# Kernel optimization log

Hardware: AMD Instinct MI355X
Metric: run time of the kernel (lower is better)

Reference implementation:

```python
import jax, jax.numpy as jnp
import numpy as np

N, D, H1, K = 4096, 128, 256, 128


def setup_inputs() -> dict:
    key = jax.random.key(0)
    ks = jax.random.split(key, 8)
    A = jax.random.uniform(ks[3], (D, D), dtype=jnp.float32)
    A = A * (1.0 - jnp.eye(D, dtype=jnp.float32))  # DAG prob mask, no self-loops
    return {
        "x": jax.random.normal(ks[0], (N, D), dtype=jnp.float32),
        "weight": jax.random.normal(ks[1], (D, D), dtype=jnp.float32) * 0.1,
        "bias": jax.random.normal(ks[2], (1, D), dtype=jnp.float32) * 0.1,
        "A": A,
        "W1": jax.random.normal(ks[4], (D, H1), dtype=jnp.float32) * 0.1,
        "b1": jax.random.normal(ks[5], (H1,), dtype=jnp.float32) * 0.1,
        "W2": jax.random.normal(ks[6], (H1, K), dtype=jnp.float32) * 0.1,
        "b2": jax.random.normal(ks[7], (K,), dtype=jnp.float32) * 0.1,
    }


def reference(x, weight, bias, A, W1, b1, W2, b2):
    # to_adj (eval path): masked weights
    W = weight * A                                   # [D, D]
    y = x @ W + bias                                 # [N, D]
    # __expand__ builds diag(y[n]) [N,D,D]; since e[n,i,:] = y[n,i]*I[i,:],
    # the first Linear collapses to a per-row scaling of W1 (same math, fused):
    # e @ W1 -> y[n,i] * W1[i,:]
    h1 = jax.nn.relu(y[:, :, None] * W1[None, :, :] + b1)   # [N, D, H1]
    f = (h1 @ W2 + b2).sum(axis=2)                   # [N, D] (sum over output dim)
    # h_func, method='gnn'
    I = jnp.eye(D, dtype=x.dtype)
    A2 = jnp.square(W)
    M = I + A2 / D
    E = jnp.linalg.matrix_power(M, D - 1)
    h_val = (E.T * M).sum() - D
    # l1_reg (same prob mask in eval)
    reg = jnp.abs(W).sum()
    return (f, h_val, reg)
```

## Files before the change

kernel.cpp:

```cpp
#include <hip/hip_runtime.h>

#define NN 4096
#define DD 128
#define HH1 256

#define WS_S    0
#define WS_S2   16384
#define WS_S3   32768
#define WS_S4   49152
#define WS_W    65536
#define WS_W2S  81920
#define WS_PAIR 82176
#define WS_B2S  82688
#define WS_TACC 82696
#define WS_DONE 82708
#define WS_REGP 82712
#define WS_WT   82944
#define WS_XT   99328
#define WS_TH   623616
#define WS_A    656384
#define WS_B    689280
#define WS_REQ_FLOATS 722176
#define WS_REQ_BYTES  (WS_REQ_FLOATS * 4UL)

#define O_S    0
#define O_S2   16384
#define O_S3   32768
#define O_S4   49152
#define O_W2S  65536
#define O_B2S  65792
#define O_TACC 65808
#define O_DONE 65824
#define O_REGP 65840

__device__ __forceinline__ float waveReduce(float v) {
#pragma unroll
  for (int off = 32; off > 0; off >>= 1) v += __shfl_down(v, off, 64);
  return v;
}


__global__ __launch_bounds__(256) void kA2(
    const float* __restrict__ weight, const float* __restrict__ Amat,
    const float* __restrict__ W2, const float* __restrict__ b2,
    const float* __restrict__ b1v, const float* __restrict__ x,
    float* __restrict__ ws) {
  const int b = blockIdx.x, tid = threadIdx.x;
  __shared__ float s_lds[DD * DD];
  __shared__ float xs[64 * 133];
  if (b < 64) {
    const float4* w4 = (const float4*)weight;
    const float4* a4 = (const float4*)Amat;
    float4* s4 = (float4*)s_lds;
    const float inv = 1.0f / 128.0f;
    for (int e = tid; e < DD * DD / 4; e += 256) {
      float4 wv = w4[e], av = a4[e], o;
      float t;
      t = wv.x * av.x; o.x = t * t * inv;
      t = wv.y * av.y; o.y = t * t * inv;
      t = wv.z * av.z; o.z = t * t * inv;
      t = wv.w * av.w; o.w = t * t * inv;
      s4[e] = o;
    }
    __syncthreads();
    const int i = (b << 1) + (tid >> 7), j = tid & 127;
    const float* row = &s_lds[i * DD];
    float acc = 0.f;
#pragma unroll 8
    for (int k = 0; k < DD; ++k) acc = fmaf(row[k], s_lds[k * DD + j], acc);
    ws[WS_S2 + i * DD + j] = acc;
  } else if (b < 72) {
    const int base = (b - 64) * 2048;
    const float inv = 1.0f / 128.0f;
    for (int e = tid; e < 2048; e += 256) {
      const int idx = base + e;
      const float w = weight[idx] * Amat[idx];
      const int k = idx >> 7, i = idx & 127;
      ws[WS_W + idx] = w;
      ws[WS_WT + i * DD + k] = w;
      ws[WS_S + idx] = w * w * inv;
    }
  } else if (b == 72) {
    const float4* r = (const float4*)(W2 + tid * 128);
    float4 s4 = make_float4(0.f, 0.f, 0.f, 0.f);
#pragma unroll 8
    for (int k = 0; k < 32; ++k) {
      const float4 v = r[k];
      s4.x += v.x; s4.y += v.y; s4.z += v.z; s4.w += v.w;
    }
    const float w2sv = (s4.x + s4.y) + (s4.z + s4.w);
    ws[WS_W2S + tid] = w2sv;
    ((float2*)(ws + WS_PAIR))[tid] = make_float2(b1v[tid], w2sv);
  } else if (b == 73) {
    __shared__ float red[4];
    float v = (tid < 128) ? b2[tid] : 0.f;
    v = waveReduce(v);
    if ((tid & 63) == 0) red[tid >> 6] = v;
    __syncthreads();
    if (tid == 0) ws[WS_B2S] = (red[0] + red[1]) + (red[2] + red[3]);
    if (tid >= 64 && tid < 74) ws[WS_TACC + (tid - 64)] = 0.f;
    if (tid == 96) *(unsigned int*)(ws + WS_DONE) = 0u;
  } else if (b < 82) {
    const int bb = b - 74;
    const int base = bb * 2048;
    float s = 0.f;
    for (int e = tid; e < 2048; e += 256) {
      const int idx = base + e;
      s += fabsf(weight[idx] * Amat[idx]);
    }
    s = waveReduce(s);
    __shared__ float red2[4];
    if ((tid & 63) == 0) red2[tid >> 6] = s;
    __syncthreads();
    if (tid == 0) ws[WS_REGP + bb] = (red2[0] + red2[1]) + (red2[2] + red2[3]);
  } else {
    const int n0 = (b - 82) * 64;
    const float4* x4 = (const float4*)x;
    for (int e = tid; e < 2048; e += 256) {
      const int r = e >> 5, c = e & 31;
      const float4 v = x4[(n0 + r) * 32 + c];
      float* p = &xs[r * 133 + (c << 2)];
      p[0] = v.x; p[1] = v.y; p[2] = v.z; p[3] = v.w;
    }
    __syncthreads();
    float* xT = ws + WS_XT;
    const int c = tid & 15, ks = tid >> 4;
#pragma unroll
    for (int m = 0; m < 8; ++m) {
      const int k = ks + (m << 4);
      float4 o;
      o.x = xs[((c << 2) + 0) * 133 + k];
      o.y = xs[((c << 2) + 1) * 133 + k];
      o.z = xs[((c << 2) + 2) * 133 + k];
      o.w = xs[((c << 2) + 3) * 133 + k];
      *(float4*)&xT[k * NN + n0 + (c << 2)] = o;
    }
  }
}

__global__ __launch_bounds__(256) void kPS(const float* __restrict__ W1,
                                           const float* __restrict__ b1v,
                                           float* __restrict__ ws) {
  const int tid = threadIdx.x;
  if (blockIdx.x < 128) {
    const int sb = blockIdx.x;
    const bool isS4 = sb >= 64;
    const int mb = isS4 ? sb - 64 : sb;
    const float* __restrict__ L = ws + WS_S2;
    const float* __restrict__ R = ws + (isS4 ? WS_S2 : WS_S);
    float* __restrict__ O = ws + (isS4 ? WS_S4 : WS_S3);
    const int i = (mb << 1) + (tid >> 7), j = tid & 127;
    float acc = 0.f;
#pragma unroll 8
    for (int k = 0; k < DD; ++k) acc = fmaf(L[i * DD + k], R[k * DD + j], acc);
    O[i * DD + j] = acc;
    return;
  }
  const int i = blockIdx.x - 128;
  __shared__ float kT[256], kS[256], kC[256];
  __shared__ float redb[8];
  __shared__ float base2[2];
  const int j = tid;
  const float w = W1[i * HH1 + j];
  const float w2s = ws[WS_W2S + j];
  const float bj = b1v[j];
  const float s = w * w2s, c = bj * w2s;
  float th, ds, dc, bs, bc;
  if (w > 0.f) {
    th = -bj / w; ds = s; dc = c; bs = 0.f; bc = 0.f;
  } else if (w < 0.f) {
    th = -bj / w; ds = -s; dc = -c; bs = s; bc = c;
  } else {
    th = 3.4e38f; ds = 0.f; dc = 0.f; bs = 0.f; bc = fmaxf(bj, 0.f) * w2s;
  }
  {
    const float rs = waveReduce(bs), rc = waveReduce(bc);
    if ((tid & 63) == 0) {
      redb[tid >> 6] = rs;
      redb[4 + (tid >> 6)] = rc;
    }
  }
  kT[tid] = th; kS[tid] = ds; kC[tid] = dc;
  __syncthreads();
  if (tid == 0) {
    base2[0] = (redb[0] + redb[1]) + (redb[2] + redb[3]);
    base2[1] = (redb[4] + redb[5]) + (redb[6] + redb[7]);
  }
  for (int kk = 2; kk <= 256; kk <<= 1) {
    for (int jj = kk >> 1; jj > 0; jj >>= 1) {
      __syncthreads();
      const int ixj = tid ^ jj;
      if (ixj > tid) {
        const bool up = ((tid & kk) == 0);
        const float ta = kT[tid], tb = kT[ixj];
        if ((ta > tb) == up) {
          kT[tid] = tb; kT[ixj] = ta;
          const float sa = kS[tid], sb = kS[ixj];
          kS[tid] = sb; kS[ixj] = sa;
          const float ca = kC[tid], cb = kC[ixj];
          kC[tid] = cb; kC[ixj] = ca;
        }
      }
    }
  }
  __syncthreads();
  for (int off = 1; off < 256; off <<= 1) {
    float vs = 0.f, vc = 0.f;
    if (tid >= off) { vs = kS[tid - off]; vc = kC[tid - off]; }
    __syncthreads();
    kS[tid] += vs; kC[tid] += vc;
    __syncthreads();
  }
  const float b_s = base2[0], b_c = base2[1];
  ws[WS_TH + i * 256 + tid] = kT[tid];
  ws[WS_A + i * 257 + tid + 1] = b_s + kS[tid];
  ws[WS_B + i * 257 + tid + 1] = b_c + kC[tid];
  if (tid == 0) {
    ws[WS_A + i * 257] = b_s;
    ws[WS_B + i * 257] = b_c;
  }
}

__global__ __launch_bounds__(256) void kC6(const float* __restrict__ bias,
                                           float* __restrict__ ws,
                                           float* __restrict__ out) {
  const int tid = threadIdx.x;
  if (blockIdx.x < 512) {
    __shared__ float lT[4 * 256];
    __shared__ float lA[4 * 257];
    __shared__ float lB[4 * 257];
    __shared__ float ts[256 * 5];
    const int fb = blockIdx.x;
    const int n0 = (fb >> 5) << 8, i0 = (fb & 31) << 2;
    const int w = tid >> 6, l = tid & 63;
    const int iu = __builtin_amdgcn_readfirstlane(i0 + w);

#pragma unroll
    for (int q = 0; q < 4; ++q) {
      lT[(q << 8) + tid] = ws[WS_TH + (i0 + q) * 256 + tid];
      lA[q * 257 + tid] = ws[WS_A + (i0 + q) * 257 + tid];
      lB[q * 257 + tid] = ws[WS_B + (i0 + q) * 257 + tid];
      if (tid == 0) {
        lA[q * 257 + 256] = ws[WS_A + (i0 + q) * 257 + 256];
        lB[q * 257 + 256] = ws[WS_B + (i0 + q) * 257 + 256];
      }
    }

    const float* __restrict__ xT = ws + WS_XT;
    const float* __restrict__ wr = ws + WS_WT + iu * DD;
    float t[4] = {0.f, 0.f, 0.f, 0.f};
#pragma unroll 8
    for (int k = 0; k < DD; ++k) {
      const float wv = wr[k];
      const float4 xv = *(const float4*)&xT[k * NN + n0 + (l << 2)];
      t[0] = fmaf(xv.x, wv, t[0]);
      t[1] = fmaf(xv.y, wv, t[1]);
      t[2] = fmaf(xv.z, wv, t[2]);
      t[3] = fmaf(xv.w, wv, t[3]);
    }
    const float bv = bias[iu];
    const float sb2 = ws[WS_B2S];
    __syncthreads();

    const float* Tw = &lT[w << 8];
    const float* Aw = &lA[w * 257];
    const float* Bw = &lB[w * 257];
#pragma unroll
    for (int q = 0; q < 4; ++q) {
      const float yq = t[q] + bv;
      int m = 0;
#pragma unroll
      for (int st = 128; st > 0; st >>= 1) {
        if (Tw[m + st - 1] <= yq) m += st;
      }
      const float f = fmaf(Aw[m], yq, Bw[m]) + sb2;
      ts[((l << 2) + q) * 5 + w] = f;
    }
    __syncthreads();
    const int m = tid;
    float4 o;
    o.x = ts[m * 5 + 0]; o.y = ts[m * 5 + 1];
    o.z = ts[m * 5 + 2]; o.w = ts[m * 5 + 3];
    *(float4*)&out[(n0 + m) * DD + i0] = o;
    return;
  }
  const int tb = blockIdx.x - 512;
  const int i = (tb << 1) + (tid >> 7), j = tid & 127;
  const float* S1 = ws + WS_S;
  const float* S2 = ws + WS_S2;
  const float* S3 = ws + WS_S3;
  const float* S4 = ws + WS_S4;
  const float a1 = S1[i * DD + j], a2 = S2[i * DD + j], a3 = S3[i * DD + j];
  const float b1t = S1[j * DD + i], b2t = S2[j * DD + i],
              b3t = S3[j * DD + i], b4t = S4[j * DD + i];
  float e7 = 0.f;
#pragma unroll 8
  for (int k = 0; k < DD; ++k) e7 = fmaf(S3[i * DD + k], S4[k * DD + j], e7);
  float c[10];
  c[0] = a1 * b1t; c[1] = a2 * b1t; c[2] = a2 * b2t; c[3] = a3 * b2t;
  c[4] = a3 * b3t; c[5] = a3 * b4t; c[6] = e7 * b1t; c[7] = e7 * b2t;
  c[8] = e7 * b3t; c[9] = e7 * b4t;
  __shared__ float red[4][10];
#pragma unroll
  for (int m = 0; m < 10; ++m) {
    const float v = waveReduce(c[m]);
    if ((tid & 63) == 0) red[tid >> 6][m] = v;
  }
  __syncthreads();
  if (tid == 0) {
    float* tacc = ws + WS_TACC;
    for (int m = 0; m < 10; ++m)
      atomicAdd(&tacc[m], (red[0][m] + red[1][m]) + (red[2][m] + red[3][m]));
    __threadfence();
    unsigned int* done = (unsigned int*)(ws + WS_DONE);
    const unsigned int old = atomicAdd(done, 1u);
    if (old == 63u) {
      __threadfence();
      double h = 0.0, C = 8128.0;
      for (int kk = 2; kk <= 11; ++kk) {
        const float tv = atomicAdd(&tacc[kk - 2], 0.0f);
        h += C * (double)tv;
        C = C * (double)(128 - kk) / (double)(kk + 1);
      }
      float reg = 0.f;
      for (int m = 0; m < 8; ++m) reg += ws[WS_REGP + m];
      out[NN * DD] = (float)h;
      out[NN * DD + 1] = reg;
    }
  }
}

__global__ __launch_bounds__(256) void kA_old(
    const float* __restrict__ weight, const float* __restrict__ Amat,
    const float* __restrict__ W2, const float* __restrict__ b2,
    float* __restrict__ ws) {
  const int b = blockIdx.x, tid = threadIdx.x;
  if (b < 64) {
    __shared__ float s_lds[DD * DD];
    const float4* w4 = (const float4*)weight;
    const float4* a4 = (const float4*)Amat;
    float4* s4 = (float4*)s_lds;
    const float inv = 1.0f / 128.0f;
    for (int e = tid; e < DD * DD / 4; e += 256) {
      float4 wv = w4[e], av = a4[e], o;
      float t;
      t = wv.x * av.x; o.x = t * t * inv;
      t = wv.y * av.y; o.y = t * t * inv;
      t = wv.z * av.z; o.z = t * t * inv;
      t = wv.w * av.w; o.w = t * t * inv;
      s4[e] = o;
    }
    __syncthreads();
    const int i = (b << 1) + (tid >> 7), j = tid & 127;
    const float* row = &s_lds[i * DD];
    float acc = 0.f;
#pragma unroll 8
    for (int k = 0; k < DD; ++k) acc = fmaf(row[k], s_lds[k * DD + j], acc);
    ws[O_S2 + i * DD + j] = acc;
  } else if (b < 72) {
    const int base = (b - 64) * 2048;
    const float inv = 1.0f / 128.0f;
    for (int e = tid; e < 2048; e += 256) {
      const int idx = base + e;
      const float w = weight[idx] * Amat[idx];
      ws[O_S + idx] = w * w * inv;
    }
  } else if (b == 72) {
    const float4* r = (const float4*)(W2 + tid * 128);
    float4 s4 = make_float4(0.f, 0.f, 0.f, 0.f);
#pragma unroll 8
    for (int k = 0; k < 32; ++k) {
      const float4 v = r[k];
      s4.x += v.x; s4.y += v.y; s4.z += v.z; s4.w += v.w;
    }
    ws[O_W2S + tid] = (s4.x + s4.y) + (s4.z + s4.w);
  } else if (b == 73) {
    __shared__ float red[4];
    float v = (tid < 128) ? b2[tid] : 0.f;
    v = waveReduce(v);
    if ((tid & 63) == 0) red[tid >> 6] = v;
    __syncthreads();
    if (tid == 0) ws[O_B2S] = (red[0] + red[1]) + (red[2] + red[3]);
    if (tid >= 64 && tid < 74) ws[O_TACC + (tid - 64)] = 0.f;
    if (tid == 96) *(unsigned int*)(ws + O_DONE) = 0u;
  } else {
    const int bb = b - 74;
    const int base = bb * 2048;
    float s = 0.f;
    for (int e = tid; e < 2048; e += 256) {
      const int idx = base + e;
      s += fabsf(weight[idx] * Amat[idx]);
    }
    s = waveReduce(s);
    __shared__ float red[4];
    if ((tid & 63) == 0) red[tid >> 6] = s;
    __syncthreads();
    if (tid == 0) ws[O_REGP + bb] = (red[0] + red[1]) + (red[2] + red[3]);
  }
}

__global__ __launch_bounds__(256) void kB_old(
    const float* __restrict__ x, const float* __restrict__ weight,
    const float* __restrict__ Amat, const float* __restrict__ bias,
    const float* __restrict__ W1, const float* __restrict__ b1v,
    float* __restrict__ ws, float* __restrict__ out) {
  const int tid = threadIdx.x;
  if (blockIdx.x < 128) {
    const int sb = blockIdx.x;
    const bool isS4 = sb >= 64;
    const int mb = isS4 ? sb - 64 : sb;
    const float* __restrict__ L = ws + O_S2;
    const float* __restrict__ R = ws + (isS4 ? O_S2 : O_S);
    float* __restrict__ O = ws + (isS4 ? O_S4 : O_S3);
    const int i = (mb << 1) + (tid >> 7), j = tid & 127;
    float acc = 0.f;
#pragma unroll 8
    for (int k = 0; k < DD; ++k) acc = fmaf(L[i * DD + k], R[k * DD + j], acc);
    O[i * DD + j] = acc;
    return;
  }
  __shared__ float xs[64 * 132];
  __shared__ float4 fq[4 * 256];
  __shared__ float wcol[4 * 128];
  __shared__ float ts[64 * 5];
  const int fb = blockIdx.x - 128;
  const int i0 = (fb & 31) << 2, n0 = (fb >> 5) << 6;
  const float4* x4 = (const float4*)x;
  for (int e = tid; e < 64 * 32; e += 256) {
    const int r = e >> 5, c = e & 31;
    *(float4*)&xs[r * 132 + (c << 2)] = x4[(n0 + r) * 32 + c];
  }
  for (int e = tid; e < 512; e += 256) {
    const int w = e >> 7, k = e & 127;
    const int gi = k * DD + i0 + w;
    wcol[(w << 7) + k] = weight[gi] * Amat[gi];
  }
  const float* w2s = ws + O_W2S;
  for (int e = tid; e < 1024; e += 256) {
    const int w = e >> 8, j = e & 255;
    fq[(w << 8) + j] = make_float4(W1[(i0 + w) * HH1 + j], b1v[j], w2s[j], 0.f);
  }
  __syncthreads();
  const int w = tid >> 6, l = tid & 63;
  float t = bias[i0 + w];
  const float4* xr = (const float4*)&xs[l * 132];
  const float4* wc = (const float4*)&wcol[w << 7];
#pragma unroll
  for (int k = 0; k < 32; ++k) {
    const float4 xv = xr[k], wv = wc[k];
    t = fmaf(xv.x, wv.x, t);
    t = fmaf(xv.y, wv.y, t);
    t = fmaf(xv.z, wv.z, t);
    t = fmaf(xv.w, wv.w, t);
  }
  float acc = ws[O_B2S];
  const float4* fp = &fq[w << 8];
#pragma unroll 8
  for (int j = 0; j < HH1; ++j) {
    const float4 c = fp[j];
    acc = fmaf(fmaxf(fmaf(t, c.x, c.y), 0.f), c.z, acc);
  }
  ts[l * 5 + w] = acc;
  __syncthreads();
  if (tid < 64) {
    const float4 o = make_float4(ts[tid * 5 + 0], ts[tid * 5 + 1],
                                 ts[tid * 5 + 2], ts[tid * 5 + 3]);
    *(float4*)&out[(n0 + tid) * DD + i0] = o;
  }
}

__global__ __launch_bounds__(256) void kC_old(float* __restrict__ ws,
                                              float* __restrict__ out) {
  const int tid = threadIdx.x;
  const int i = (blockIdx.x << 1) + (tid >> 7), j = tid & 127;
  const float* S1 = ws + O_S;
  const float* S2 = ws + O_S2;
  const float* S3 = ws + O_S3;
  const float* S4 = ws + O_S4;
  const float a1 = S1[i * DD + j], a2 = S2[i * DD + j], a3 = S3[i * DD + j];
  const float b1t = S1[j * DD + i], b2t = S2[j * DD + i],
              b3t = S3[j * DD + i], b4t = S4[j * DD + i];
  float e7 = 0.f;
#pragma unroll 8
  for (int k = 0; k < DD; ++k) e7 = fmaf(S3[i * DD + k], S4[k * DD + j], e7);
  float c[10];
  c[0] = a1 * b1t; c[1] = a2 * b1t; c[2] = a2 * b2t; c[3] = a3 * b2t;
  c[4] = a3 * b3t; c[5] = a3 * b4t; c[6] = e7 * b1t; c[7] = e7 * b2t;
  c[8] = e7 * b3t; c[9] = e7 * b4t;
  __shared__ float red[4][10];
#pragma unroll
  for (int m = 0; m < 10; ++m) {
    const float v = waveReduce(c[m]);
    if ((tid & 63) == 0) red[tid >> 6][m] = v;
  }
  __syncthreads();
  if (tid == 0) {
    float* tacc = ws + O_TACC;
    for (int m = 0; m < 10; ++m)
      atomicAdd(&tacc[m], (red[0][m] + red[1][m]) + (red[2][m] + red[3][m]));
    __threadfence();
    unsigned int* done = (unsigned int*)(ws + O_DONE);
    const unsigned int old = atomicAdd(done, 1u);
    if (old == 63u) {
      __threadfence();
      double h = 0.0, C = 8128.0;
      for (int kk = 2; kk <= 11; ++kk) {
        const float tv = atomicAdd(&tacc[kk - 2], 0.0f);
        h += C * (double)tv;
        C = C * (double)(128 - kk) / (double)(kk + 1);
      }
      float reg = 0.f;
      for (int m = 0; m < 8; ++m) reg += ws[O_REGP + m];
      out[NN * DD] = (float)h;
      out[NN * DD + 1] = reg;
    }
  }
}

extern "C" void kernel_launch(void* const* d_in, const int* in_sizes, int n_in,
                              void* d_out, int out_size, void* d_ws,
                              size_t ws_size, hipStream_t stream) {
  const float* x      = (const float*)d_in[0];
  const float* weight = (const float*)d_in[1];
  const float* bias   = (const float*)d_in[2];
  const float* Amat   = (const float*)d_in[3];
  const float* W1     = (const float*)d_in[4];
  const float* b1v    = (const float*)d_in[5];
  const float* W2     = (const float*)d_in[6];
  const float* b2     = (const float*)d_in[7];
  float* out = (float*)d_out;
  float* ws  = (float*)d_ws;

  if (ws_size >= WS_REQ_BYTES) {
    kA2<<<146, 256, 0, stream>>>(weight, Amat, W2, b2, b1v, x, ws);
    kPS<<<256, 256, 0, stream>>>(W1, b1v, ws);
    kC6<<<576, 256, 0, stream>>>(bias, ws, out);
  } else {
    kA_old<<<82, 256, 0, stream>>>(weight, Amat, W2, b2, ws);
    kB_old<<<128 + 2048, 256, 0, stream>>>(x, weight, Amat, bias, W1, b1v, ws,
                                           out);
    kC_old<<<64, 256, 0, stream>>>(ws, out);
  }
}
```

Baseline: 116.5 us.

## Move threshold sort blocks into first kernel, recomputing W2 row sums per block

The per-row threshold sort and prefix-scan blocks move from the second kernel into the first. Each block now computes the W2 row sums itself rather than reading them from workspace, so it no longer waits on a prior kernel. The second kernel keeps only the S3/S4 matrix products. The x-transpose staging buffer now reuses the shared s_lds array, which cuts the first kernel's LDS footprint. The cost is redundant W2 reads in 128 blocks and a larger first grid, with a shorter critical path in the second kernel.

```diff
diff --git a/kernel.cpp b/kernel.cpp
--- a/kernel.cpp
+++ b/kernel.cpp
@@ -40,14 +40,13 @@
 }
 
 
-__global__ __launch_bounds__(256) void kA2(
+__global__ __launch_bounds__(256) void kA3(
     const float* __restrict__ weight, const float* __restrict__ Amat,
     const float* __restrict__ W2, const float* __restrict__ b2,
     const float* __restrict__ b1v, const float* __restrict__ x,
-    float* __restrict__ ws) {
+    const float* __restrict__ W1, float* __restrict__ ws) {
   const int b = blockIdx.x, tid = threadIdx.x;
   __shared__ float s_lds[DD * DD];
-  __shared__ float xs[64 * 133];
   if (b < 64) {
     const float4* w4 = (const float4*)weight;
     const float4* a4 = (const float4*)Amat;
@@ -81,17 +80,6 @@
       ws[WS_S + idx] = w * w * inv;
     }
   } else if (b == 72) {
-    const float4* r = (const float4*)(W2 + tid * 128);
-    float4 s4 = make_float4(0.f, 0.f, 0.f, 0.f);
-#pragma unroll 8
-    for (int k = 0; k < 32; ++k) {
-      const float4 v = r[k];
-      s4.x += v.x; s4.y += v.y; s4.z += v.z; s4.w += v.w;
-    }
-    const float w2sv = (s4.x + s4.y) + (s4.z + s4.w);
-    ws[WS_W2S + tid] = w2sv;
-    ((float2*)(ws + WS_PAIR))[tid] = make_float2(b1v[tid], w2sv);
-  } else if (b == 73) {
     __shared__ float red[4];
     float v = (tid < 128) ? b2[tid] : 0.f;
     v = waveReduce(v);
@@ -100,8 +88,8 @@
     if (tid == 0) ws[WS_B2S] = (red[0] + red[1]) + (red[2] + red[3]);
     if (tid >= 64 && tid < 74) ws[WS_TACC + (tid - 64)] = 0.f;
     if (tid == 96) *(unsigned int*)(ws + WS_DONE) = 0u;
-  } else if (b < 82) {
-    const int bb = b - 74;
+  } else if (b < 81) {
+    const int bb = b - 73;
     const int base = bb * 2048;
     float s = 0.f;
     for (int e = tid; e < 2048; e += 256) {
@@ -113,8 +101,9 @@
     if ((tid & 63) == 0) red2[tid >> 6] = s;
     __syncthreads();
     if (tid == 0) ws[WS_REGP + bb] = (red2[0] + red2[1]) + (red2[2] + red2[3]);
-  } else {
-    const int n0 = (b - 82) * 64;
+  } else if (b < 145) {
+    float* xs = s_lds;
+    const int n0 = (b - 81) * 64;
     const float4* x4 = (const float4*)x;
     for (int e = tid; e < 2048; e += 256) {
       const int r = e >> 5, c = e & 31;
@@ -135,90 +124,95 @@
       o.w = xs[((c << 2) + 3) * 133 + k];
       *(float4*)&xT[k * NN + n0 + (c << 2)] = o;
     }
-  }
-}
-
-__global__ __launch_bounds__(256) void kPS(const float* __restrict__ W1,
-                                           const float* __restrict__ b1v,
-                                           float* __restrict__ ws) {
-  const int tid = threadIdx.x;
-  if (blockIdx.x < 128) {
-    const int sb = blockIdx.x;
-    const bool isS4 = sb >= 64;
-    const int mb = isS4 ? sb - 64 : sb;
-    const float* __restrict__ L = ws + WS_S2;
-    const float* __restrict__ R = ws + (isS4 ? WS_S2 : WS_S);
-    float* __restrict__ O = ws + (isS4 ? WS_S4 : WS_S3);
-    const int i = (mb << 1) + (tid >> 7), j = tid & 127;
-    float acc = 0.f;
-#pragma unroll 8
-    for (int k = 0; k < DD; ++k) acc = fmaf(L[i * DD + k], R[k * DD + j], acc);
-    O[i * DD + j] = acc;
-    return;
-  }
-  const int i = blockIdx.x - 128;
-  __shared__ float kT[256], kS[256], kC[256];
-  __shared__ float redb[8];
-  __shared__ float base2[2];
-  const int j = tid;
-  const float w = W1[i * HH1 + j];
-  const float w2s = ws[WS_W2S + j];
-  const float bj = b1v[j];
-  const float s = w * w2s, c = bj * w2s;
-  float th, ds, dc, bs, bc;
-  if (w > 0.f) {
-    th = -bj / w; ds = s; dc = c; bs = 0.f; bc = 0.f;
-  } else if (w < 0.f) {
-    th = -bj / w; ds = -s; dc = -c; bs = s; bc = c;
   } else {
-    th = 3.4e38f; ds = 0.f; dc = 0.f; bs = 0.f; bc = fmaxf(bj, 0.f) * w2s;
-  }
-  {
-    const float rs = waveReduce(bs), rc = waveReduce(bc);
-    if ((tid & 63) == 0) {
-      redb[tid >> 6] = rs;
-      redb[4 + (tid >> 6)] = rc;
-    }
-  }
-  kT[tid] = th; kS[tid] = ds; kC[tid] = dc;
-  __syncthreads();
-  if (tid == 0) {
-    base2[0] = (redb[0] + redb[1]) + (redb[2] + redb[3]);
-    base2[1] = (redb[4] + redb[5]) + (redb[6] + redb[7]);
-  }
-  for (int kk = 2; kk <= 256; kk <<= 1) {
-    for (int jj = kk >> 1; jj > 0; jj >>= 1) {
-      __syncthreads();
-      const int ixj = tid ^ jj;
-      if (ixj > tid) {
-        const bool up = ((tid & kk) == 0);
-        const float ta = kT[tid], tb = kT[ixj];
-        if ((ta > tb) == up) {
-          kT[tid] = tb; kT[ixj] = ta;
-          const float sa = kS[tid], sb = kS[ixj];
-          kS[tid] = sb; kS[ixj] = sa;
-          const float ca = kC[tid], cb = kC[ixj];
-          kC[tid] = cb; kC[ixj] = ca;
+    const int i = b - 145;
+    float* kT = s_lds;
+    float* kS = s_lds + 256;
+    float* kC = s_lds + 512;
+    __shared__ float redb[8];
+    __shared__ float base2[2];
+    const int j = tid;
+    const float4* r = (const float4*)(W2 + j * 128);
+    float4 s4v = make_float4(0.f, 0.f, 0.f, 0.f);
+#pragma unroll 8
+    for (int k = 0; k < 32; ++k) {
+      const float4 v = r[k];
+      s4v.x += v.x; s4v.y += v.y; s4v.z += v.z; s4v.w += v.w;
+    }
+    const float w2s = (s4v.x + s4v.y) + (s4v.z + s4v.w);
+    const float w = W1[i * HH1 + j];
+    const float bj = b1v[j];
+    const float s = w * w2s, c = bj * w2s;
+    float th, ds, dc, bs, bc;
+    if (w > 0.f) {
+      th = -bj / w; ds = s; dc = c; bs = 0.f; bc = 0.f;
+    } else if (w < 0.f) {
+      th = -bj / w; ds = -s; dc = -c; bs = s; bc = c;
+    } else {
+      th = 3.4e38f; ds = 0.f; dc = 0.f; bs = 0.f; bc = fmaxf(bj, 0.f) * w2s;
+    }
+    {
+      const float rs = waveReduce(bs), rc = waveReduce(bc);
+      if ((tid & 63) == 0) {
+        redb[tid >> 6] = rs;
+        redb[4 + (tid >> 6)] = rc;
+      }
+    }
+    kT[tid] = th; kS[tid] = ds; kC[tid] = dc;
+    __syncthreads();
+    if (tid == 0) {
+      base2[0] = (redb[0] + redb[1]) + (redb[2] + redb[3]);
+      base2[1] = (redb[4] + redb[5]) + (redb[6] + redb[7]);
+    }
+    for (int kk = 2; kk <= 256; kk <<= 1) {
+      for (int jj = kk >> 1; jj > 0; jj >>= 1) {
+        __syncthreads();
+        const int ixj = tid ^ jj;
+        if (ixj > tid) {
+          const bool up = ((tid & kk) == 0);
+          const float ta = kT[tid], tb = kT[ixj];
+          if ((ta > tb) == up) {
+            kT[tid] = tb; kT[ixj] = ta;
+            const float sa = kS[tid], sb = kS[ixj];
+            kS[tid] = sb; kS[ixj] = sa;
+            const float ca = kC[tid], cb = kC[ixj];
+            kC[tid] = cb; kC[ixj] = ca;
+          }
         }
       }
     }
-  }
-  __syncthreads();
-  for (int off = 1; off < 256; off <<= 1) {
-    float vs = 0.f, vc = 0.f;
-    if (tid >= off) { vs = kS[tid - off]; vc = kC[tid - off]; }
-    __syncthreads();
-    kS[tid] += vs; kC[tid] += vc;
-    __syncthreads();
-  }
-  const float b_s = base2[0], b_c = base2[1];
-  ws[WS_TH + i * 256 + tid] = kT[tid];
-  ws[WS_A + i * 257 + tid + 1] = b_s + kS[tid];
-  ws[WS_B + i * 257 + tid + 1] = b_c + kC[tid];
-  if (tid == 0) {
-    ws[WS_A + i * 257] = b_s;
-    ws[WS_B + i * 257] = b_c;
-  }
+    __syncthreads();
+    for (int off = 1; off < 256; off <<= 1) {
+      float vs = 0.f, vc = 0.f;
+      if (tid >= off) { vs = kS[tid - off]; vc = kC[tid - off]; }
+      __syncthreads();
+      kS[tid] += vs; kC[tid] += vc;
+      __syncthreads();
+    }
+    const float b_s = base2[0], b_c = base2[1];
+    ws[WS_TH + i * 256 + tid] = kT[tid];
+    ws[WS_A + i * 257 + tid + 1] = b_s + kS[tid];
+    ws[WS_B + i * 257 + tid + 1] = b_c + kC[tid];
+    if (tid == 0) {
+      ws[WS_A + i * 257] = b_s;
+      ws[WS_B + i * 257] = b_c;
+    }
+  }
+}
+
+__global__ __launch_bounds__(256) void kS34(float* __restrict__ ws) {
+  const int tid = threadIdx.x;
+  const int sb = blockIdx.x;
+  const bool isS4 = sb >= 64;
+  const int mb = isS4 ? sb - 64 : sb;
+  const float* __restrict__ L = ws + WS_S2;
+  const float* __restrict__ R = ws + (isS4 ? WS_S2 : WS_S);
+  float* __restrict__ O = ws + (isS4 ? WS_S4 : WS_S3);
+  const int i = (mb << 1) + (tid >> 7), j = tid & 127;
+  float acc = 0.f;
+#pragma unroll 8
+  for (int k = 0; k < DD; ++k) acc = fmaf(L[i * DD + k], R[k * DD + j], acc);
+  O[i * DD + j] = acc;
 }
 
 __global__ __launch_bounds__(256) void kC6(const float* __restrict__ bias,
@@ -532,8 +526,8 @@
   float* ws  = (float*)d_ws;
 
   if (ws_size >= WS_REQ_BYTES) {
-    kA2<<<146, 256, 0, stream>>>(weight, Amat, W2, b2, b1v, x, ws);
-    kPS<<<256, 256, 0, stream>>>(W1, b1v, ws);
+    kA3<<<273, 256, 0, stream>>>(weight, Amat, W2, b2, b1v, x, W1, ws);
+    kS34<<<128, 256, 0, stream>>>(ws);
     kC6<<<576, 256, 0, stream>>>(bias, ws, out);
   } else {
     kA_old<<<82, 256, 0, stream>>>(weight, Amat, W2, b2, ws);
```

Result: slower. 124.3 us (+6.7%).
